# Optimization experiments

Measured on AMD Instinct MI355X. Metric: run time of the kernel, lower is better.

The kernel has to match this reference:

```python
import jax, jax.numpy as jnp
import numpy as np

N_USER = 100000
N_ITEM = 100000
N_EDGE = 1600000
HID = 64
IN_U = 128
IN_I = 64
N_LAYERS = 2


def setup_inputs() -> dict:
    key = jax.random.key(0)
    ks = jax.random.split(key, 12)
    s = 0.05
    return {
        "x_user": jax.random.normal(ks[0], (N_USER, IN_U), jnp.float32),
        "x_item": jax.random.normal(ks[1], (N_ITEM, IN_I), jnp.float32),
        "edge_ui": jax.random.randint(ks[2], (2, N_EDGE), 0, N_USER),  # row0 src(user), row1 dst(item)
        "edge_iu": jax.random.randint(ks[3], (2, N_EDGE), 0, N_ITEM),  # row0 src(item), row1 dst(user)
        "Wu": jax.random.normal(ks[4], (IN_U, HID), jnp.float32) * s,
        "bu": jnp.zeros((HID,), jnp.float32),
        "Wi": jax.random.normal(ks[5], (IN_I, HID), jnp.float32) * s,
        "bi": jnp.zeros((HID,), jnp.float32),
        "Wl": jax.random.normal(ks[6], (N_LAYERS, 2, HID, HID), jnp.float32) * s,
        "bl": jnp.zeros((N_LAYERS, 2, HID), jnp.float32),
        "Wr": jax.random.normal(ks[7], (N_LAYERS, 2, HID, HID), jnp.float32) * s,
    }


def _sage(h_src, h_dst, edge, Wl, bl, Wr, n_dst):
    # SAGEConv: mean-aggregate gathered source features, then lin_l(agg)+bias + lin_r(dst)
    src, dst = edge[0], edge[1]
    msg = h_src[src]  # [E, HID] gather
    agg = jax.ops.segment_sum(msg, dst, num_segments=n_dst)
    cnt = jax.ops.segment_sum(jnp.ones((edge.shape[1], 1), h_src.dtype), dst, num_segments=n_dst)
    mean = agg / jnp.maximum(cnt, 1.0)
    return mean @ Wl + bl + h_dst @ Wr


def reference(x_user, x_item, edge_ui, edge_iu, Wu, bu, Wi, bi, Wl, bl, Wr):
    # per-node-type input linear + relu (dropout = identity at inference)
    hu = jax.nn.relu(x_user @ Wu + bu)
    hi = jax.nn.relu(x_item @ Wi + bi)
    for l in range(N_LAYERS):
        # edge type 0: user -> item ; edge type 1: item -> user ; HeteroConv aggr='sum'
        new_i = _sage(hu, hi, edge_ui, Wl[l, 0], bl[l, 0], Wr[l, 0], N_ITEM)
        new_u = _sage(hi, hu, edge_iu, Wl[l, 1], bl[l, 1], Wr[l, 1], N_USER)
        hu = jax.nn.relu(new_u)
        hi = jax.nn.relu(new_i)
    return hu, hi
```

## Files before the change

### kernel.cpp

```cpp
#include <hip/hip_runtime.h>

#define NUSER 100000
#define NITEM 100000
#define NEDGE 1600000
#define HID 64
#define NPB 256
#define NBKT 391
#define ACHUNK 8192
#define NCHUNK ((NEDGE + ACHUNK - 1) / ACHUNK)

typedef float f32x4 __attribute__((ext_vector_type(4)));

__device__ __forceinline__ unsigned short f2bf(float x) {
  unsigned int u; __builtin_memcpy(&u, &x, 4);
  u += 0x7fffu + ((u >> 16) & 1u);
  return (unsigned short)(u >> 16);
}
__device__ __forceinline__ float bflo(unsigned int u) {
  unsigned int v = u << 16; float f; __builtin_memcpy(&f, &v, 4); return f;
}
__device__ __forceinline__ float bfhi(unsigned int u) {
  unsigned int v = u & 0xffff0000u; float f; __builtin_memcpy(&f, &v, 4); return f;
}

template<int K>
__global__ __launch_bounds__(256) void gemm64(
    const float* __restrict__ A, const float* __restrict__ W,
    const float* __restrict__ bias, float* __restrict__ C, int M)
{
  __shared__ float Ws[K * 64];
  __shared__ float As[64 * 68];
  const int tid = threadIdx.x;

  for (int i = tid; i < K * 16; i += 256)
    ((float4*)Ws)[i] = ((const float4*)W)[i];

  const int tx = tid & 15;
  const int ty = tid >> 4;
  float4 bv = ((const float4*)bias)[tx];

  const int ntiles = (M + 63) >> 6;
  for (int t = blockIdx.x; t < ntiles; t += gridDim.x) {
    const int row0 = t << 6;
    float acc[4][4] = {};
    for (int kb = 0; kb < K; kb += 64) {
      __syncthreads();
      for (int i = tid; i < 1024; i += 256) {
        int r = i >> 4;
        int kk = (i & 15) << 2;
        int gr = row0 + r; if (gr > M - 1) gr = M - 1;
        *(float4*)&As[r * 68 + kk] = *(const float4*)(A + (size_t)gr * K + kb + kk);
      }
      __syncthreads();
      #pragma unroll 8
      for (int k = 0; k < 64; ++k) {
        float4 w = *(const float4*)&Ws[(kb + k) * 64 + tx * 4];
        float a0 = As[(ty * 4 + 0) * 68 + k];
        float a1 = As[(ty * 4 + 1) * 68 + k];
        float a2 = As[(ty * 4 + 2) * 68 + k];
        float a3 = As[(ty * 4 + 3) * 68 + k];
        acc[0][0] += a0 * w.x; acc[0][1] += a0 * w.y; acc[0][2] += a0 * w.z; acc[0][3] += a0 * w.w;
        acc[1][0] += a1 * w.x; acc[1][1] += a1 * w.y; acc[1][2] += a1 * w.z; acc[1][3] += a1 * w.w;
        acc[2][0] += a2 * w.x; acc[2][1] += a2 * w.y; acc[2][2] += a2 * w.z; acc[2][3] += a2 * w.w;
        acc[3][0] += a3 * w.x; acc[3][1] += a3 * w.y; acc[3][2] += a3 * w.z; acc[3][3] += a3 * w.w;
      }
    }
    #pragma unroll
    for (int r = 0; r < 4; ++r) {
      int gr = row0 + ty * 4 + r;
      if (gr < M) {
        float4 o = make_float4(fmaxf(acc[r][0] + bv.x, 0.f), fmaxf(acc[r][1] + bv.y, 0.f),
                               fmaxf(acc[r][2] + bv.z, 0.f), fmaxf(acc[r][3] + bv.w, 0.f));
        *(float4*)(C + (size_t)gr * 64 + tx * 4) = o;
      }
    }
  }
}

__global__ __launch_bounds__(256) void gemm_dual2(
    const float* A0, const float* __restrict__ Wa0, const float* __restrict__ Wb0,
    const float* __restrict__ bias0, unsigned short* Ga0, float* Tb0,
    const float* A1, const float* __restrict__ Wa1, const float* __restrict__ Wb1,
    const float* __restrict__ bias1, unsigned short* Ga1, float* Tb1,
    int M, int half_blocks)
{
  __shared__ float Ws[64 * 128];
  __shared__ float As[64 * 68];
  const int tid = threadIdx.x;

  const float* A; const float* Wa; const float* Wb; const float* bias;
  unsigned short* Ga; float* Tb; int t;
  if ((int)blockIdx.x < half_blocks) {
    A = A0; Wa = Wa0; Wb = Wb0; bias = bias0; Ga = Ga0; Tb = Tb0; t = blockIdx.x;
  } else {
    A = A1; Wa = Wa1; Wb = Wb1; bias = bias1; Ga = Ga1; Tb = Tb1; t = blockIdx.x - half_blocks;
  }

  for (int i = tid; i < 2048; i += 256) {
    int k = i >> 5, cg = i & 31;
    float4 v = (cg < 16) ? ((const float4*)Wa)[k * 16 + cg]
                         : ((const float4*)Wb)[k * 16 + (cg - 16)];
    ((float4*)Ws)[k * 32 + cg] = v;
  }

  const int tx = tid & 15;
  const int ty = tid >> 4;
  float4 bvB = ((const float4*)bias)[tx];

  const int row0 = t << 6;
  float accA[4][4] = {};
  float accB[4][4] = {};
  __syncthreads();
  for (int i = tid; i < 1024; i += 256) {
    int r = i >> 4;
    int kk = (i & 15) << 2;
    int gr = row0 + r; if (gr > M - 1) gr = M - 1;
    *(float4*)&As[r * 68 + kk] = *(const float4*)(A + (size_t)gr * 64 + kk);
  }
  __syncthreads();
  #pragma unroll 8
  for (int k = 0; k < 64; ++k) {
    float4 wa = *(const float4*)&Ws[k * 128 + tx * 4];
    float4 wb = *(const float4*)&Ws[k * 128 + 64 + tx * 4];
    float a0 = As[(ty * 4 + 0) * 68 + k];
    float a1 = As[(ty * 4 + 1) * 68 + k];
    float a2 = As[(ty * 4 + 2) * 68 + k];
    float a3 = As[(ty * 4 + 3) * 68 + k];
    accA[0][0] += a0 * wa.x; accA[0][1] += a0 * wa.y; accA[0][2] += a0 * wa.z; accA[0][3] += a0 * wa.w;
    accA[1][0] += a1 * wa.x; accA[1][1] += a1 * wa.y; accA[1][2] += a1 * wa.z; accA[1][3] += a1 * wa.w;
    accA[2][0] += a2 * wa.x; accA[2][1] += a2 * wa.y; accA[2][2] += a2 * wa.z; accA[2][3] += a2 * wa.w;
    accA[3][0] += a3 * wa.x; accA[3][1] += a3 * wa.y; accA[3][2] += a3 * wa.z; accA[3][3] += a3 * wa.w;
    accB[0][0] += a0 * wb.x; accB[0][1] += a0 * wb.y; accB[0][2] += a0 * wb.z; accB[0][3] += a0 * wb.w;
    accB[1][0] += a1 * wb.x; accB[1][1] += a1 * wb.y; accB[1][2] += a1 * wb.z; accB[1][3] += a1 * wb.w;
    accB[2][0] += a2 * wb.x; accB[2][1] += a2 * wb.y; accB[2][2] += a2 * wb.z; accB[2][3] += a2 * wb.w;
    accB[3][0] += a3 * wb.x; accB[3][1] += a3 * wb.y; accB[3][2] += a3 * wb.z; accB[3][3] += a3 * wb.w;
  }
  #pragma unroll
  for (int r = 0; r < 4; ++r) {
    int gr = row0 + ty * 4 + r;
    if (gr < M) {
      ushort4 g;
      g.x = f2bf(accA[r][0]); g.y = f2bf(accA[r][1]);
      g.z = f2bf(accA[r][2]); g.w = f2bf(accA[r][3]);
      *(ushort4*)(Ga + (size_t)gr * 64 + tx * 4) = g;
      *(float4*)(Tb + (size_t)gr * 64 + tx * 4) =
          make_float4(accB[r][0] + bvB.x, accB[r][1] + bvB.y,
                      accB[r][2] + bvB.z, accB[r][3] + bvB.w);
    }
  }
}

__global__ __launch_bounds__(256) void agg2(
    const unsigned short* __restrict__ G0, const float* T0,
    const int* __restrict__ ptr0, const int* __restrict__ idx0, float* out0,
    const unsigned short* __restrict__ G1, const float* T1,
    const int* __restrict__ ptr1, const int* __restrict__ idx1, float* out1,
    int n_dst)
{
  const int lane = threadIdx.x & 63;
  const int sub = lane >> 5;
  const int s32 = lane & 31;
  const int k = s32 >> 4;
  const int c4 = (s32 & 15) << 2;
  int wave = blockIdx.x * 4 + (threadIdx.x >> 6);
  const int nwh = (gridDim.x * 4) >> 1;
  const unsigned short* G; const float* T; const int* ptr; const int* idx; float* out;
  if (wave < nwh) { G = G0; T = T0; ptr = ptr0; idx = idx0; out = out0; }
  else { G = G1; T = T1; ptr = ptr1; idx = idx1; out = out1; wave -= nwh; }

  for (int n0 = wave * 2; n0 < n_dst; n0 += nwh * 2) {
    const int n = n0 + sub;
    if (n >= n_dst) continue;
    const int s = ptr[n];
    const int e = ptr[n + 1];
    f32x4 t = {};
    if (k == 0)
      t = __builtin_nontemporal_load((const f32x4*)(T + (size_t)n * 64 + c4));
    float a0 = 0.f, a1 = 0.f, a2 = 0.f, a3 = 0.f;
    int i = s;
    for (; i + 16 <= e; i += 16) {
      int j0 = __builtin_nontemporal_load(idx + i + 0  + k);
      int j1 = __builtin_nontemporal_load(idx + i + 2  + k);
      int j2 = __builtin_nontemporal_load(idx + i + 4  + k);
      int j3 = __builtin_nontemporal_load(idx + i + 6  + k);
      int j4 = __builtin_nontemporal_load(idx + i + 8  + k);
      int j5 = __builtin_nontemporal_load(idx + i + 10 + k);
      int j6 = __builtin_nontemporal_load(idx + i + 12 + k);
      int j7 = __builtin_nontemporal_load(idx + i + 14 + k);
      uint2 g0 = *(const uint2*)(G + (size_t)j0 * 64 + c4);
      uint2 g1 = *(const uint2*)(G + (size_t)j1 * 64 + c4);
      uint2 g2 = *(const uint2*)(G + (size_t)j2 * 64 + c4);
      uint2 g3 = *(const uint2*)(G + (size_t)j3 * 64 + c4);
      uint2 g4 = *(const uint2*)(G + (size_t)j4 * 64 + c4);
      uint2 g5 = *(const uint2*)(G + (size_t)j5 * 64 + c4);
      uint2 g6 = *(const uint2*)(G + (size_t)j6 * 64 + c4);
      uint2 g7 = *(const uint2*)(G + (size_t)j7 * 64 + c4);
      a0 += bflo(g0.x); a1 += bfhi(g0.x); a2 += bflo(g0.y); a3 += bfhi(g0.y);
      a0 += bflo(g1.x); a1 += bfhi(g1.x); a2 += bflo(g1.y); a3 += bfhi(g1.y);
      a0 += bflo(g2.x); a1 += bfhi(g2.x); a2 += bflo(g2.y); a3 += bfhi(g2.y);
      a0 += bflo(g3.x); a1 += bfhi(g3.x); a2 += bflo(g3.y); a3 += bfhi(g3.y);
      a0 += bflo(g4.x); a1 += bfhi(g4.x); a2 += bflo(g4.y); a3 += bfhi(g4.y);
      a0 += bflo(g5.x); a1 += bfhi(g5.x); a2 += bflo(g5.y); a3 += bfhi(g5.y);
      a0 += bflo(g6.x); a1 += bfhi(g6.x); a2 += bflo(g6.y); a3 += bfhi(g6.y);
      a0 += bflo(g7.x); a1 += bfhi(g7.x); a2 += bflo(g7.y); a3 += bfhi(g7.y);
    }
    if (i < e) {
      const int em1 = e - 1;
      const int t0 = i + 0  + k, t1 = i + 2  + k, t2 = i + 4  + k, t3 = i + 6  + k;
      const int t4 = i + 8  + k, t5 = i + 10 + k, t6 = i + 12 + k, t7 = i + 14 + k;
      int j0 = __builtin_nontemporal_load(idx + min(t0, em1));
      int j1 = __builtin_nontemporal_load(idx + min(t1, em1));
      int j2 = __builtin_nontemporal_load(idx + min(t2, em1));
      int j3 = __builtin_nontemporal_load(idx + min(t3, em1));
      int j4 = __builtin_nontemporal_load(idx + min(t4, em1));
      int j5 = __builtin_nontemporal_load(idx + min(t5, em1));
      int j6 = __builtin_nontemporal_load(idx + min(t6, em1));
      int j7 = __builtin_nontemporal_load(idx + min(t7, em1));
      uint2 g0 = *(const uint2*)(G + (size_t)j0 * 64 + c4);
      uint2 g1 = *(const uint2*)(G + (size_t)j1 * 64 + c4);
      uint2 g2 = *(const uint2*)(G + (size_t)j2 * 64 + c4);
      uint2 g3 = *(const uint2*)(G + (size_t)j3 * 64 + c4);
      uint2 g4 = *(const uint2*)(G + (size_t)j4 * 64 + c4);
      uint2 g5 = *(const uint2*)(G + (size_t)j5 * 64 + c4);
      uint2 g6 = *(const uint2*)(G + (size_t)j6 * 64 + c4);
      uint2 g7 = *(const uint2*)(G + (size_t)j7 * 64 + c4);
      float w0 = (t0 <= em1) ? 1.f : 0.f;
      float w1 = (t1 <= em1) ? 1.f : 0.f;
      float w2 = (t2 <= em1) ? 1.f : 0.f;
      float w3 = (t3 <= em1) ? 1.f : 0.f;
      float w4 = (t4 <= em1) ? 1.f : 0.f;
      float w5 = (t5 <= em1) ? 1.f : 0.f;
      float w6 = (t6 <= em1) ? 1.f : 0.f;
      float w7 = (t7 <= em1) ? 1.f : 0.f;
      a0 = fmaf(bflo(g0.x), w0, a0); a1 = fmaf(bfhi(g0.x), w0, a1);
      a2 = fmaf(bflo(g0.y), w0, a2); a3 = fmaf(bfhi(g0.y), w0, a3);
      a0 = fmaf(bflo(g1.x), w1, a0); a1 = fmaf(bfhi(g1.x), w1, a1);
      a2 = fmaf(bflo(g1.y), w1, a2); a3 = fmaf(bfhi(g1.y), w1, a3);
      a0 = fmaf(bflo(g2.x), w2, a0); a1 = fmaf(bfhi(g2.x), w2, a1);
      a2 = fmaf(bflo(g2.y), w2, a2); a3 = fmaf(bfhi(g2.y), w2, a3);
      a0 = fmaf(bflo(g3.x), w3, a0); a1 = fmaf(bfhi(g3.x), w3, a1);
      a2 = fmaf(bflo(g3.y), w3, a2); a3 = fmaf(bfhi(g3.y), w3, a3);
      a0 = fmaf(bflo(g4.x), w4, a0); a1 = fmaf(bfhi(g4.x), w4, a1);
      a2 = fmaf(bflo(g4.y), w4, a2); a3 = fmaf(bfhi(g4.y), w4, a3);
      a0 = fmaf(bflo(g5.x), w5, a0); a1 = fmaf(bfhi(g5.x), w5, a1);
      a2 = fmaf(bflo(g5.y), w5, a2); a3 = fmaf(bfhi(g5.y), w5, a3);
      a0 = fmaf(bflo(g6.x), w6, a0); a1 = fmaf(bfhi(g6.x), w6, a1);
      a2 = fmaf(bflo(g6.y), w6, a2); a3 = fmaf(bfhi(g6.y), w6, a3);
      a0 = fmaf(bflo(g7.x), w7, a0); a1 = fmaf(bfhi(g7.x), w7, a1);
      a2 = fmaf(bflo(g7.y), w7, a2); a3 = fmaf(bfhi(g7.y), w7, a3);
    }
    a0 += __shfl_xor(a0, 16);
    a1 += __shfl_xor(a1, 16);
    a2 += __shfl_xor(a2, 16);
    a3 += __shfl_xor(a3, 16);
    const int deg = e - s;
    const float inv = 1.f / (float)(deg > 0 ? deg : 1);
    if (k == 0) {
      f32x4 o;
      o.x = fmaxf(fmaf(a0, inv, t.x), 0.f);
      o.y = fmaxf(fmaf(a1, inv, t.y), 0.f);
      o.z = fmaxf(fmaf(a2, inv, t.z), 0.f);
      o.w = fmaxf(fmaf(a3, inv, t.w), 0.f);
      __builtin_nontemporal_store(o, (f32x4*)(out + (size_t)n * 64 + c4));
    }
  }
}

__global__ __launch_bounds__(256) void bucket_hist(
    const int* __restrict__ dstA, const int* __restrict__ dstB,
    int* histA, int* histB, int E)
{
  __shared__ int h[NBKT];
  for (int i = threadIdx.x; i < NBKT; i += 256) h[i] = 0;
  __syncthreads();
  const int half = gridDim.x >> 1;
  const bool isB = (int)blockIdx.x >= half;
  const int* dst = isB ? dstB : dstA;
  int* hist = isB ? histB : histA;
  const int b0 = isB ? blockIdx.x - half : blockIdx.x;
  for (int e = b0 * 256 + (int)threadIdx.x; e < E; e += half * 256)
    atomicAdd(&h[__builtin_nontemporal_load(dst + e) >> 8], 1);
  __syncthreads();
  for (int i = threadIdx.x; i < NBKT; i += 256)
    if (h[i]) atomicAdd(&hist[i], h[i]);
}

__global__ __launch_bounds__(512) void bucket_scan(
    const int* __restrict__ histA, const int* __restrict__ histB,
    int* baseA, int* curA, int* baseB, int* curB,
    int* ptrA_end, int* ptrB_end, int E)
{
  __shared__ int sA[512], sB[512];
  const int t = threadIdx.x;
  int vA = (t < NBKT) ? histA[t] : 0;
  int vB = (t < NBKT) ? histB[t] : 0;
  sA[t] = vA; sB[t] = vB;
  __syncthreads();
  for (int off = 1; off < 512; off <<= 1) {
    int xA = 0, xB = 0;
    if (t >= off) { xA = sA[t - off]; xB = sB[t - off]; }
    __syncthreads();
    if (t >= off) { sA[t] += xA; sB[t] += xB; }
    __syncthreads();
  }
  if (t < NBKT) {
    int eA = sA[t] - vA, eB = sB[t] - vB;
    baseA[t] = eA; curA[t] = eA;
    baseB[t] = eB; curB[t] = eB;
  }
  if (t == 0) {
    baseA[NBKT] = E; baseB[NBKT] = E;
    *ptrA_end = E; *ptrB_end = E;
  }
}

__global__ __launch_bounds__(256) void partition2(
    const int* __restrict__ srcA, const int* __restrict__ dstA, int* curA, unsigned int* pairsA,
    const int* __restrict__ srcB, const int* __restrict__ dstB, int* curB, unsigned int* pairsB,
    int E)
{
  __shared__ int h[NBKT];
  __shared__ int c[NBKT];
  const int half = gridDim.x >> 1;
  const bool isB = (int)blockIdx.x >= half;
  const int chunk = isB ? blockIdx.x - half : blockIdx.x;
  const int* src = isB ? srcB : srcA;
  const int* dst = isB ? dstB : dstA;
  int* cur = isB ? curB : curA;
  unsigned int* pairs = isB ? pairsB : pairsA;
  const int e0 = chunk * ACHUNK;
  const int e1 = min(e0 + ACHUNK, E);
  for (int i = threadIdx.x; i < NBKT; i += 256) h[i] = 0;
  __syncthreads();
  for (int e = e0 + (int)threadIdx.x; e < e1; e += 256)
    atomicAdd(&h[__builtin_nontemporal_load(dst + e) >> 8], 1);
  __syncthreads();
  for (int i = threadIdx.x; i < NBKT; i += 256) {
    int v = h[i];
    if (v) c[i] = atomicAdd(&cur[i], v);
  }
  __syncthreads();
  for (int e = e0 + (int)threadIdx.x; e < e1; e += 256) {
    int d = __builtin_nontemporal_load(dst + e);
    int s = __builtin_nontemporal_load(src + e);
    int b = d >> 8;
    int p = atomicAdd(&c[b], 1);
    pairs[p] = ((unsigned int)(d & 255) << 24) | (unsigned int)s;
  }
}

__global__ __launch_bounds__(256) void bucket_fill(
    const unsigned int* __restrict__ pairsA, const int* __restrict__ baseA,
    int* __restrict__ ptrA, int* __restrict__ idxA,
    const unsigned int* __restrict__ pairsB, const int* __restrict__ baseB,
    int* __restrict__ ptrB, int* __restrict__ idxB, int n)
{
  __shared__ int h[NPB];
  __shared__ int cur[NPB];
  const bool isB = (int)blockIdx.x >= NBKT;
  const int b = isB ? blockIdx.x - NBKT : blockIdx.x;
  const unsigned int* pairs = isB ? pairsB : pairsA;
  const int* base = isB ? baseB : baseA;
  int* ptr = isB ? ptrB : ptrA;
  int* idx = isB ? idxB : idxA;
  const int ebase = base[b];
  const int eend = base[b + 1];
  const int t = threadIdx.x;
  h[t] = 0;
  __syncthreads();
  for (int e = ebase + t; e < eend; e += 256)
    atomicAdd(&h[pairs[e] >> 24], 1);
  __syncthreads();
  const int v = h[t];
  __syncthreads();
  for (int off = 1; off < 256; off <<= 1) {
    int x = 0;
    if (t >= off) x = h[t - off];
    __syncthreads();
    if (t >= off) h[t] += x;
    __syncthreads();
  }
  const int excl = h[t] - v;
  const int gnode = b * NPB + t;
  if (gnode < n) ptr[gnode] = ebase + excl;
  cur[t] = excl;
  __syncthreads();
  for (int e = ebase + t; e < eend; e += 256) {
    unsigned int pk = pairs[e];
    int p = atomicAdd(&cur[pk >> 24], 1);
    idx[ebase + p] = (int)(pk & 0xFFFFFFu);
  }
}

extern "C" void kernel_launch(void* const* d_in, const int* in_sizes, int n_in,
                              void* d_out, int out_size, void* d_ws, size_t ws_size,
                              hipStream_t stream) {
  const float* x_user = (const float*)d_in[0];
  const float* x_item = (const float*)d_in[1];
  const int*   edge_ui = (const int*)d_in[2];
  const int*   edge_iu = (const int*)d_in[3];
  const float* Wu = (const float*)d_in[4];
  const float* bu = (const float*)d_in[5];
  const float* Wi = (const float*)d_in[6];
  const float* bi = (const float*)d_in[7];
  const float* Wl = (const float*)d_in[8];
  const float* bl = (const float*)d_in[9];
  const float* Wr = (const float*)d_in[10];

  float* outU = (float*)d_out;
  float* outI = outU + (size_t)NUSER * HID;

  char* p = (char*)d_ws;
  auto alloc = [&](size_t bytes) -> void* {
    void* r = (void*)p; p += (bytes + 255) & ~(size_t)255; return r;
  };
  float* U = (float*)alloc((size_t)NUSER * HID * 4);
  float* I = (float*)alloc((size_t)NITEM * HID * 4);
  unsigned short* GA = (unsigned short*)alloc((size_t)NUSER * HID * 2);
  unsigned short* GB = (unsigned short*)alloc((size_t)NITEM * HID * 2);
  unsigned int* pairsA = (unsigned int*)GA;
  unsigned int* pairsB = pairsA + NEDGE;
  int* histA = (int*)alloc((size_t)(2 * NBKT + 2 * (NBKT + 1) + 2 * NBKT) * 4);
  int* histB = histA + NBKT;
  int* baseA = histB + NBKT;
  int* baseB = baseA + NBKT + 1;
  int* curA  = baseB + NBKT + 1;
  int* curB  = curA + NBKT;
  int* ptr_ui = (int*)alloc(((size_t)NITEM + 1) * 4);
  int* ptr_iu = (int*)alloc(((size_t)NUSER + 1) * 4);
  int* idx_ui = (int*)alloc((size_t)NEDGE * 4);
  int* idx_iu = (int*)alloc((size_t)NEDGE * 4);

  hipError_t _e = hipMemsetAsync(histA, 0, (size_t)(2 * NBKT) * 4, stream); (void)_e;
  bucket_hist<<<784, 256, 0, stream>>>(edge_ui + NEDGE, edge_iu + NEDGE,
                                       histA, histB, NEDGE);
  bucket_scan<<<1, 512, 0, stream>>>(histA, histB, baseA, curA, baseB, curB,
                                     ptr_ui + NITEM, ptr_iu + NUSER, NEDGE);
  partition2<<<2 * NCHUNK, 256, 0, stream>>>(
      edge_ui, edge_ui + NEDGE, curA, pairsA,
      edge_iu, edge_iu + NEDGE, curB, pairsB, NEDGE);
  bucket_fill<<<2 * NBKT, 256, 0, stream>>>(pairsA, baseA, ptr_ui, idx_ui,
                                            pairsB, baseB, ptr_iu, idx_iu, NITEM);

  const int GT = (NUSER + 63) / 64;
  const int AGG_B = 2560;

  const float* Wl00 = Wl;             const float* Wl01 = Wl + 4096;
  const float* Wl10 = Wl + 2 * 4096;  const float* Wl11 = Wl + 3 * 4096;
  const float* Wr00 = Wr;             const float* Wr01 = Wr + 4096;
  const float* Wr10 = Wr + 2 * 4096;  const float* Wr11 = Wr + 3 * 4096;
  const float* bl00 = bl;             const float* bl01 = bl + 64;
  const float* bl10 = bl + 128;       const float* bl11 = bl + 192;

  gemm64<128><<<GT, 256, 0, stream>>>(x_user, Wu, bu, U, NUSER);
  gemm64<64 ><<<GT, 256, 0, stream>>>(x_item, Wi, bi, I, NITEM);

  gemm_dual2<<<2 * GT, 256, 0, stream>>>(U, Wl00, Wr01, bl01, GA, outU,
                                         I, Wl01, Wr00, bl00, GB, outI,
                                         NUSER, GT);
  agg2<<<AGG_B, 256, 0, stream>>>(GA, outI, ptr_ui, idx_ui, outI,
                                  GB, outU, ptr_iu, idx_iu, outU, NITEM);

  gemm_dual2<<<2 * GT, 256, 0, stream>>>(outI, Wl11, Wr10, bl10, GA, outI,
                                         outU, Wl10, Wr11, bl11, GB, outU,
                                         NITEM, GT);
  agg2<<<AGG_B, 256, 0, stream>>>(GA, outU, ptr_iu, idx_iu, outU,
                                  GB, outI, ptr_ui, idx_ui, outI, NUSER);
}
```

Before: 568.6 us.

## Quantize gathered neighbor features to int8 with per-row scales

The GEMM epilogue now writes each row of the aggregated-branch projection as unsigned 8-bit values with a per-row float scale, instead of bf16. The aggregation kernel gathers 4-byte packed codes plus the scale and dequantizes with fmas, then applies a 128*sum-of-scales offset correction before the mean. This halves the bytes fetched per random neighbor gather, at the cost of an extra scale load per edge and lower precision. The aggregation grid is also resized to roughly one node pair per wave.

```diff
diff --git a/kernel.cpp b/kernel.cpp
--- a/kernel.cpp
+++ b/kernel.cpp
@@ -10,18 +10,6 @@
 #define NCHUNK ((NEDGE + ACHUNK - 1) / ACHUNK)
 
 typedef float f32x4 __attribute__((ext_vector_type(4)));
-
-__device__ __forceinline__ unsigned short f2bf(float x) {
-  unsigned int u; __builtin_memcpy(&u, &x, 4);
-  u += 0x7fffu + ((u >> 16) & 1u);
-  return (unsigned short)(u >> 16);
-}
-__device__ __forceinline__ float bflo(unsigned int u) {
-  unsigned int v = u << 16; float f; __builtin_memcpy(&f, &v, 4); return f;
-}
-__device__ __forceinline__ float bfhi(unsigned int u) {
-  unsigned int v = u & 0xffff0000u; float f; __builtin_memcpy(&f, &v, 4); return f;
-}
 
 template<int K>
 __global__ __launch_bounds__(256) void gemm64(
@@ -79,9 +67,9 @@
 
 __global__ __launch_bounds__(256) void gemm_dual2(
     const float* A0, const float* __restrict__ Wa0, const float* __restrict__ Wb0,
-    const float* __restrict__ bias0, unsigned short* Ga0, float* Tb0,
+    const float* __restrict__ bias0, unsigned char* Ga0, float* Gs0, float* Tb0,
     const float* A1, const float* __restrict__ Wa1, const float* __restrict__ Wb1,
-    const float* __restrict__ bias1, unsigned short* Ga1, float* Tb1,
+    const float* __restrict__ bias1, unsigned char* Ga1, float* Gs1, float* Tb1,
     int M, int half_blocks)
 {
   __shared__ float Ws[64 * 128];
@@ -89,11 +77,11 @@
   const int tid = threadIdx.x;
 
   const float* A; const float* Wa; const float* Wb; const float* bias;
-  unsigned short* Ga; float* Tb; int t;
+  unsigned char* Ga; float* Gs; float* Tb; int t;
   if ((int)blockIdx.x < half_blocks) {
-    A = A0; Wa = Wa0; Wb = Wb0; bias = bias0; Ga = Ga0; Tb = Tb0; t = blockIdx.x;
+    A = A0; Wa = Wa0; Wb = Wb0; bias = bias0; Ga = Ga0; Gs = Gs0; Tb = Tb0; t = blockIdx.x;
   } else {
-    A = A1; Wa = Wa1; Wb = Wb1; bias = bias1; Ga = Ga1; Tb = Tb1; t = blockIdx.x - half_blocks;
+    A = A1; Wa = Wa1; Wb = Wb1; bias = bias1; Ga = Ga1; Gs = Gs1; Tb = Tb1; t = blockIdx.x - half_blocks;
   }
 
   for (int i = tid; i < 2048; i += 256) {
@@ -137,12 +125,23 @@
   }
   #pragma unroll
   for (int r = 0; r < 4; ++r) {
+    float m = fmaxf(fmaxf(fabsf(accA[r][0]), fabsf(accA[r][1])),
+                    fmaxf(fabsf(accA[r][2]), fabsf(accA[r][3])));
+    m = fmaxf(m, __shfl_xor(m, 1));
+    m = fmaxf(m, __shfl_xor(m, 2));
+    m = fmaxf(m, __shfl_xor(m, 4));
+    m = fmaxf(m, __shfl_xor(m, 8));
+    const float s = m * (1.f / 127.f);
+    const float inv = (m > 0.f) ? 127.f / m : 0.f;
     int gr = row0 + ty * 4 + r;
     if (gr < M) {
-      ushort4 g;
-      g.x = f2bf(accA[r][0]); g.y = f2bf(accA[r][1]);
-      g.z = f2bf(accA[r][2]); g.w = f2bf(accA[r][3]);
-      *(ushort4*)(Ga + (size_t)gr * 64 + tx * 4) = g;
+      unsigned int q0 = (unsigned int)((int)rintf(accA[r][0] * inv) + 128);
+      unsigned int q1 = (unsigned int)((int)rintf(accA[r][1] * inv) + 128);
+      unsigned int q2 = (unsigned int)((int)rintf(accA[r][2] * inv) + 128);
+      unsigned int q3 = (unsigned int)((int)rintf(accA[r][3] * inv) + 128);
+      *(unsigned int*)(Ga + (size_t)gr * 64 + tx * 4) =
+          q0 | (q1 << 8) | (q2 << 16) | (q3 << 24);
+      if (tx == 0) Gs[gr] = s;
       *(float4*)(Tb + (size_t)gr * 64 + tx * 4) =
           make_float4(accB[r][0] + bvB.x, accB[r][1] + bvB.y,
                       accB[r][2] + bvB.z, accB[r][3] + bvB.w);
@@ -151,9 +150,9 @@
 }
 
 __global__ __launch_bounds__(256) void agg2(
-    const unsigned short* __restrict__ G0, const float* T0,
+    const unsigned char* __restrict__ G0, const float* __restrict__ S0, const float* T0,
     const int* __restrict__ ptr0, const int* __restrict__ idx0, float* out0,
-    const unsigned short* __restrict__ G1, const float* T1,
+    const unsigned char* __restrict__ G1, const float* __restrict__ S1, const float* T1,
     const int* __restrict__ ptr1, const int* __restrict__ idx1, float* out1,
     int n_dst)
 {
@@ -164,9 +163,10 @@
   const int c4 = (s32 & 15) << 2;
   int wave = blockIdx.x * 4 + (threadIdx.x >> 6);
   const int nwh = (gridDim.x * 4) >> 1;
-  const unsigned short* G; const float* T; const int* ptr; const int* idx; float* out;
-  if (wave < nwh) { G = G0; T = T0; ptr = ptr0; idx = idx0; out = out0; }
-  else { G = G1; T = T1; ptr = ptr1; idx = idx1; out = out1; wave -= nwh; }
+  const unsigned char* G; const float* S; const float* T;
+  const int* ptr; const int* idx; float* out;
+  if (wave < nwh) { G = G0; S = S0; T = T0; ptr = ptr0; idx = idx0; out = out0; }
+  else { G = G1; S = S1; T = T1; ptr = ptr1; idx = idx1; out = out1; wave -= nwh; }
 
   for (int n0 = wave * 2; n0 < n_dst; n0 += nwh * 2) {
     const int n = n0 + sub;
@@ -176,7 +176,7 @@
     f32x4 t = {};
     if (k == 0)
       t = __builtin_nontemporal_load((const f32x4*)(T + (size_t)n * 64 + c4));
-    float a0 = 0.f, a1 = 0.f, a2 = 0.f, a3 = 0.f;
+    float a0 = 0.f, a1 = 0.f, a2 = 0.f, a3 = 0.f, ssum = 0.f;
     int i = s;
     for (; i + 16 <= e; i += 16) {
       int j0 = __builtin_nontemporal_load(idx + i + 0  + k);
@@ -187,22 +187,33 @@
       int j5 = __builtin_nontemporal_load(idx + i + 10 + k);
       int j6 = __builtin_nontemporal_load(idx + i + 12 + k);
       int j7 = __builtin_nontemporal_load(idx + i + 14 + k);
-      uint2 g0 = *(const uint2*)(G + (size_t)j0 * 64 + c4);
-      uint2 g1 = *(const uint2*)(G + (size_t)j1 * 64 + c4);
-      uint2 g2 = *(const uint2*)(G + (size_t)j2 * 64 + c4);
-      uint2 g3 = *(const uint2*)(G + (size_t)j3 * 64 + c4);
-      uint2 g4 = *(const uint2*)(G + (size_t)j4 * 64 + c4);
-      uint2 g5 = *(const uint2*)(G + (size_t)j5 * 64 + c4);
-      uint2 g6 = *(const uint2*)(G + (size_t)j6 * 64 + c4);
-      uint2 g7 = *(const uint2*)(G + (size_t)j7 * 64 + c4);
-      a0 += bflo(g0.x); a1 += bfhi(g0.x); a2 += bflo(g0.y); a3 += bfhi(g0.y);
-      a0 += bflo(g1.x); a1 += bfhi(g1.x); a2 += bflo(g1.y); a3 += bfhi(g1.y);
-      a0 += bflo(g2.x); a1 += bfhi(g2.x); a2 += bflo(g2.y); a3 += bfhi(g2.y);
-      a0 += bflo(g3.x); a1 += bfhi(g3.x); a2 += bflo(g3.y); a3 += bfhi(g3.y);
-      a0 += bflo(g4.x); a1 += bfhi(g4.x); a2 += bflo(g4.y); a3 += bfhi(g4.y);
-      a0 += bflo(g5.x); a1 += bfhi(g5.x); a2 += bflo(g5.y); a3 += bfhi(g5.y);
-      a0 += bflo(g6.x); a1 += bfhi(g6.x); a2 += bflo(g6.y); a3 += bfhi(g6.y);
-      a0 += bflo(g7.x); a1 += bfhi(g7.x); a2 += bflo(g7.y); a3 += bfhi(g7.y);
+      float s0 = S[j0]; float s1 = S[j1]; float s2 = S[j2]; float s3 = S[j3];
+      float s4 = S[j4]; float s5 = S[j5]; float s6 = S[j6]; float s7 = S[j7];
+      unsigned int g0 = *(const unsigned int*)(G + (size_t)j0 * 64 + c4);
+      unsigned int g1 = *(const unsigned int*)(G + (size_t)j1 * 64 + c4);
+      unsigned int g2 = *(const unsigned int*)(G + (size_t)j2 * 64 + c4);
+      unsigned int g3 = *(const unsigned int*)(G + (size_t)j3 * 64 + c4);
+      unsigned int g4 = *(const unsigned int*)(G + (size_t)j4 * 64 + c4);
+      unsigned int g5 = *(const unsigned int*)(G + (size_t)j5 * 64 + c4);
+      unsigned int g6 = *(const unsigned int*)(G + (size_t)j6 * 64 + c4);
+      unsigned int g7 = *(const unsigned int*)(G + (size_t)j7 * 64 + c4);
+      a0 = fmaf((float)(g0 & 255u), s0, a0); a1 = fmaf((float)((g0 >> 8) & 255u), s0, a1);
+      a2 = fmaf((float)((g0 >> 16) & 255u), s0, a2); a3 = fmaf((float)(g0 >> 24), s0, a3);
+      a0 = fmaf((float)(g1 & 255u), s1, a0); a1 = fmaf((float)((g1 >> 8) & 255u), s1, a1);
+      a2 = fmaf((float)((g1 >> 16) & 255u), s1, a2); a3 = fmaf((float)(g1 >> 24), s1, a3);
+      a0 = fmaf((float)(g2 & 255u), s2, a0); a1 = fmaf((float)((g2 >> 8) & 255u), s2, a1);
+      a2 = fmaf((float)((g2 >> 16) & 255u), s2, a2); a3 = fmaf((float)(g2 >> 24), s2, a3);
+      a0 = fmaf((float)(g3 & 255u), s3, a0); a1 = fmaf((float)((g3 >> 8) & 255u), s3, a1);
+      a2 = fmaf((float)((g3 >> 16) & 255u), s3, a2); a3 = fmaf((float)(g3 >> 24), s3, a3);
+      a0 = fmaf((float)(g4 & 255u), s4, a0); a1 = fmaf((float)((g4 >> 8) & 255u), s4, a1);
+      a2 = fmaf((float)((g4 >> 16) & 255u), s4, a2); a3 = fmaf((float)(g4 >> 24), s4, a3);
+      a0 = fmaf((float)(g5 & 255u), s5, a0); a1 = fmaf((float)((g5 >> 8) & 255u), s5, a1);
+      a2 = fmaf((float)((g5 >> 16) & 255u), s5, a2); a3 = fmaf((float)(g5 >> 24), s5, a3);
+      a0 = fmaf((float)(g6 & 255u), s6, a0); a1 = fmaf((float)((g6 >> 8) & 255u), s6, a1);
+      a2 = fmaf((float)((g6 >> 16) & 255u), s6, a2); a3 = fmaf((float)(g6 >> 24), s6, a3);
+      a0 = fmaf((float)(g7 & 255u), s7, a0); a1 = fmaf((float)((g7 >> 8) & 255u), s7, a1);
+      a2 = fmaf((float)((g7 >> 16) & 255u), s7, a2); a3 = fmaf((float)(g7 >> 24), s7, a3);
+      ssum += ((s0 + s1) + (s2 + s3)) + ((s4 + s5) + (s6 + s7));
     }
     if (i < e) {
       const int em1 = e - 1;
@@ -216,51 +227,54 @@
       int j5 = __builtin_nontemporal_load(idx + min(t5, em1));
       int j6 = __builtin_nontemporal_load(idx + min(t6, em1));
       int j7 = __builtin_nontemporal_load(idx + min(t7, em1));
-      uint2 g0 = *(const uint2*)(G + (size_t)j0 * 64 + c4);
-      uint2 g1 = *(const uint2*)(G + (size_t)j1 * 64 + c4);
-      uint2 g2 = *(const uint2*)(G + (size_t)j2 * 64 + c4);
-      uint2 g3 = *(const uint2*)(G + (size_t)j3 * 64 + c4);
-      uint2 g4 = *(const uint2*)(G + (size_t)j4 * 64 + c4);
-      uint2 g5 = *(const uint2*)(G + (size_t)j5 * 64 + c4);
-      uint2 g6 = *(const uint2*)(G + (size_t)j6 * 64 + c4);
-      uint2 g7 = *(const uint2*)(G + (size_t)j7 * 64 + c4);
-      float w0 = (t0 <= em1) ? 1.f : 0.f;
-      float w1 = (t1 <= em1) ? 1.f : 0.f;
-      float w2 = (t2 <= em1) ? 1.f : 0.f;
-      float w3 = (t3 <= em1) ? 1.f : 0.f;
-      float w4 = (t4 <= em1) ? 1.f : 0.f;
-      float w5 = (t5 <= em1) ? 1.f : 0.f;
-      float w6 = (t6 <= em1) ? 1.f : 0.f;
-      float w7 = (t7 <= em1) ? 1.f : 0.f;
-      a0 = fmaf(bflo(g0.x), w0, a0); a1 = fmaf(bfhi(g0.x), w0, a1);
-      a2 = fmaf(bflo(g0.y), w0, a2); a3 = fmaf(bfhi(g0.y), w0, a3);
-      a0 = fmaf(bflo(g1.x), w1, a0); a1 = fmaf(bfhi(g1.x), w1, a1);
-      a2 = fmaf(bflo(g1.y), w1, a2); a3 = fmaf(bfhi(g1.y), w1, a3);
-      a0 = fmaf(bflo(g2.x), w2, a0); a1 = fmaf(bfhi(g2.x), w2, a1);
-      a2 = fmaf(bflo(g2.y), w2, a2); a3 = fmaf(bfhi(g2.y), w2, a3);
-      a0 = fmaf(bflo(g3.x), w3, a0); a1 = fmaf(bfhi(g3.x), w3, a1);
-      a2 = fmaf(bflo(g3.y), w3, a2); a3 = fmaf(bfhi(g3.y), w3, a3);
-      a0 = fmaf(bflo(g4.x), w4, a0); a1 = fmaf(bfhi(g4.x), w4, a1);
-      a2 = fmaf(bflo(g4.y), w4, a2); a3 = fmaf(bfhi(g4.y), w4, a3);
-      a0 = fmaf(bflo(g5.x), w5, a0); a1 = fmaf(bfhi(g5.x), w5, a1);
-      a2 = fmaf(bflo(g5.y), w5, a2); a3 = fmaf(bfhi(g5.y), w5, a3);
-      a0 = fmaf(bflo(g6.x), w6, a0); a1 = fmaf(bfhi(g6.x), w6, a1);
-      a2 = fmaf(bflo(g6.y), w6, a2); a3 = fmaf(bfhi(g6.y), w6, a3);
-      a0 = fmaf(bflo(g7.x), w7, a0); a1 = fmaf(bfhi(g7.x), w7, a1);
-      a2 = fmaf(bflo(g7.y), w7, a2); a3 = fmaf(bfhi(g7.y), w7, a3);
+      float s0 = (t0 <= em1) ? S[j0] : 0.f;
+      float s1 = (t1 <= em1) ? S[j1] : 0.f;
+      float s2 = (t2 <= em1) ? S[j2] : 0.f;
+      float s3 = (t3 <= em1) ? S[j3] : 0.f;
+      float s4 = (t4 <= em1) ? S[j4] : 0.f;
+      float s5 = (t5 <= em1) ? S[j5] : 0.f;
+      float s6 = (t6 <= em1) ? S[j6] : 0.f;
+      float s7 = (t7 <= em1) ? S[j7] : 0.f;
+      unsigned int g0 = *(const unsigned int*)(G + (size_t)j0 * 64 + c4);
+      unsigned int g1 = *(const unsigned int*)(G + (size_t)j1 * 64 + c4);
+      unsigned int g2 = *(const unsigned int*)(G + (size_t)j2 * 64 + c4);
+      unsigned int g3 = *(const unsigned int*)(G + (size_t)j3 * 64 + c4);
+      unsigned int g4 = *(const unsigned int*)(G + (size_t)j4 * 64 + c4);
+      unsigned int g5 = *(const unsigned int*)(G + (size_t)j5 * 64 + c4);
+      unsigned int g6 = *(const unsigned int*)(G + (size_t)j6 * 64 + c4);
+      unsigned int g7 = *(const unsigned int*)(G + (size_t)j7 * 64 + c4);
+      a0 = fmaf((float)(g0 & 255u), s0, a0); a1 = fmaf((float)((g0 >> 8) & 255u), s0, a1);
+      a2 = fmaf((float)((g0 >> 16) & 255u), s0, a2); a3 = fmaf((float)(g0 >> 24), s0, a3);
+      a0 = fmaf((float)(g1 & 255u), s1, a0); a1 = fmaf((float)((g1 >> 8) & 255u), s1, a1);
+      a2 = fmaf((float)((g1 >> 16) & 255u), s1, a2); a3 = fmaf((float)(g1 >> 24), s1, a3);
+      a0 = fmaf((float)(g2 & 255u), s2, a0); a1 = fmaf((float)((g2 >> 8) & 255u), s2, a1);
+      a2 = fmaf((float)((g2 >> 16) & 255u), s2, a2); a3 = fmaf((float)(g2 >> 24), s2, a3);
+      a0 = fmaf((float)(g3 & 255u), s3, a0); a1 = fmaf((float)((g3 >> 8) & 255u), s3, a1);
+      a2 = fmaf((float)((g3 >> 16) & 255u), s3, a2); a3 = fmaf((float)(g3 >> 24), s3, a3);
+      a0 = fmaf((float)(g4 & 255u), s4, a0); a1 = fmaf((float)((g4 >> 8) & 255u), s4, a1);
+      a2 = fmaf((float)((g4 >> 16) & 255u), s4, a2); a3 = fmaf((float)(g4 >> 24), s4, a3);
+      a0 = fmaf((float)(g5 & 255u), s5, a0); a1 = fmaf((float)((g5 >> 8) & 255u), s5, a1);
+      a2 = fmaf((float)((g5 >> 16) & 255u), s5, a2); a3 = fmaf((float)(g5 >> 24), s5, a3);
+      a0 = fmaf((float)(g6 & 255u), s6, a0); a1 = fmaf((float)((g6 >> 8) & 255u), s6, a1);
+      a2 = fmaf((float)((g6 >> 16) & 255u), s6, a2); a3 = fmaf((float)(g6 >> 24), s6, a3);
+      a0 = fmaf((float)(g7 & 255u), s7, a0); a1 = fmaf((float)((g7 >> 8) & 255u), s7, a1);
+      a2 = fmaf((float)((g7 >> 16) & 255u), s7, a2); a3 = fmaf((float)(g7 >> 24), s7, a3);
+      ssum += ((s0 + s1) + (s2 + s3)) + ((s4 + s5) + (s6 + s7));
     }
     a0 += __shfl_xor(a0, 16);
     a1 += __shfl_xor(a1, 16);
     a2 += __shfl_xor(a2, 16);
     a3 += __shfl_xor(a3, 16);
+    ssum += __shfl_xor(ssum, 16);
     const int deg = e - s;
     const float inv = 1.f / (float)(deg > 0 ? deg : 1);
     if (k == 0) {
+      const float corr = 128.f * ssum;
       f32x4 o;
-      o.x = fmaxf(fmaf(a0, inv, t.x), 0.f);
-      o.y = fmaxf(fmaf(a1, inv, t.y), 0.f);
-      o.z = fmaxf(fmaf(a2, inv, t.z), 0.f);
-      o.w = fmaxf(fmaf(a3, inv, t.w), 0.f);
+      o.x = fmaxf(fmaf(a0 - corr, inv, t.x), 0.f);
+      o.y = fmaxf(fmaf(a1 - corr, inv, t.y), 0.f);
+      o.z = fmaxf(fmaf(a2 - corr, inv, t.z), 0.f);
+      o.w = fmaxf(fmaf(a3 - corr, inv, t.w), 0.f);
       __builtin_nontemporal_store(o, (f32x4*)(out + (size_t)n * 64 + c4));
     }
   }
@@ -416,10 +430,12 @@
   };
   float* U = (float*)alloc((size_t)NUSER * HID * 4);
   float* I = (float*)alloc((size_t)NITEM * HID * 4);
-  unsigned short* GA = (unsigned short*)alloc((size_t)NUSER * HID * 2);
-  unsigned short* GB = (unsigned short*)alloc((size_t)NITEM * HID * 2);
+  unsigned char* GA = (unsigned char*)alloc((size_t)NUSER * HID);
+  unsigned char* GB = (unsigned char*)alloc((size_t)NITEM * HID);
+  float* GsA = (float*)alloc((size_t)NUSER * 4);
+  float* GsB = (float*)alloc((size_t)NITEM * 4);
   unsigned int* pairsA = (unsigned int*)GA;
-  unsigned int* pairsB = pairsA + NEDGE;
+  unsigned int* pairsB = (unsigned int*)GB;
   int* histA = (int*)alloc((size_t)(2 * NBKT + 2 * (NBKT + 1) + 2 * NBKT) * 4);
   int* histB = histA + NBKT;
   int* baseA = histB + NBKT;
@@ -443,7 +459,7 @@
                                             pairsB, baseB, ptr_iu, idx_iu, NITEM);
 
   const int GT = (NUSER + 63) / 64;
-  const int AGG_B = 2560;
+  const int AGG_B = 2 * ((NUSER / 2 + 3) / 4);
 
   const float* Wl00 = Wl;             const float* Wl01 = Wl + 4096;
   const float* Wl10 = Wl + 2 * 4096;  const float* Wl11 = Wl + 3 * 4096;
@@ -455,15 +471,15 @@
   gemm64<128><<<GT, 256, 0, stream>>>(x_user, Wu, bu, U, NUSER);
   gemm64<64 ><<<GT, 256, 0, stream>>>(x_item, Wi, bi, I, NITEM);
 
-  gemm_dual2<<<2 * GT, 256, 0, stream>>>(U, Wl00, Wr01, bl01, GA, outU,
-                                         I, Wl01, Wr00, bl00, GB, outI,
+  gemm_dual2<<<2 * GT, 256, 0, stream>>>(U, Wl00, Wr01, bl01, GA, GsA, outU,
+                                         I, Wl01, Wr00, bl00, GB, GsB, outI,
                                          NUSER, GT);
-  agg2<<<AGG_B, 256, 0, stream>>>(GA, outI, ptr_ui, idx_ui, outI,
-                                  GB, outU, ptr_iu, idx_iu, outU, NITEM);
-
-  gemm_dual2<<<2 * GT, 256, 0, stream>>>(outI, Wl11, Wr10, bl10, GA, outI,
-                                         outU, Wl10, Wr11, bl11, GB, outU,
+  agg2<<<AGG_B, 256, 0, stream>>>(GA, GsA, outI, ptr_ui, idx_ui, outI,
+                                  GB, GsB, outU, ptr_iu, idx_iu, outU, NITEM);
+
+  gemm_dual2<<<2 * GT, 256, 0, stream>>>(outI, Wl11, Wr10, bl10, GA, GsA, outI,
+                                         outU, Wl10, Wr11, bl11, GB, GsB, outU,
                                          NITEM, GT);
-  agg2<<<AGG_B, 256, 0, stream>>>(GA, outU, ptr_iu, idx_iu, outU,
-                                  GB, outI, ptr_ui, idx_ui, outI, NUSER);
-}
+  agg2<<<AGG_B, 256, 0, stream>>>(GA, GsA, outU, ptr_iu, idx_iu, outU,
+                                  GB, GsB, outI, ptr_ui, idx_ui, outI, NUSER);
+}
```

Result: no change. 578.0 us (+1.7%).
